# Performance work log

Measured on AMD Instinct MI355X. Metric: run time of the kernel, lower is better.

The kernel has to match this reference:

```python
import jax, jax.numpy as jnp
import numpy as np

N = 50000      # nodes
E = 640000     # edges (before self loops)
IN = 128       # in_channels
H = 4          # heads (layer 1)
C = 64         # hidden_channels per head
OUT = 64       # out_channels
SLOPE = 0.2    # PyG GATConv default negative_slope


def setup_inputs() -> dict:
    key = jax.random.key(0)
    ks = jax.random.split(key, 12)
    x = jax.random.normal(ks[0], (N, IN), dtype=jnp.float32)
    edge_src = jax.random.randint(ks[1], (E,), 0, N, dtype=jnp.int32)
    edge_dst = jax.random.randint(ks[2], (E,), 0, N, dtype=jnp.int32)
    # Layer 1 params: Linear IN -> H*C, attention vectors a_src/a_dst [H, C], bias [H*C]
    W1 = jax.random.normal(ks[3], (IN, H * C), dtype=jnp.float32) / np.sqrt(IN)
    att_src1 = jax.random.normal(ks[4], (H, C), dtype=jnp.float32) / np.sqrt(C)
    att_dst1 = jax.random.normal(ks[5], (H, C), dtype=jnp.float32) / np.sqrt(C)
    b1 = jnp.zeros((H * C,), dtype=jnp.float32)
    # Layer 2 params: Linear H*C -> OUT, 1 head
    W2 = jax.random.normal(ks[6], (H * C, OUT), dtype=jnp.float32) / np.sqrt(H * C)
    att_src2 = jax.random.normal(ks[7], (1, OUT), dtype=jnp.float32) / np.sqrt(OUT)
    att_dst2 = jax.random.normal(ks[8], (1, OUT), dtype=jnp.float32) / np.sqrt(OUT)
    b2 = jnp.zeros((OUT,), dtype=jnp.float32)
    return {"x": x, "W1": W1, "att_src1": att_src1, "att_dst1": att_dst1, "b1": b1,
            "W2": W2, "att_src2": att_src2, "att_dst2": att_dst2, "b2": b2,
            "edge_src": edge_src, "edge_dst": edge_dst}


def gat_conv(x, src, dst, W, a_src, a_dst, b, heads, ch):
    """PyG GATConv (concat=True): gather -> LeakyReLU attention -> per-dst softmax -> scatter-add."""
    n = x.shape[0]
    h = (x @ W).reshape(n, heads, ch)                  # [N, H, C]
    al_s = jnp.sum(h * a_src, axis=-1)                 # [N, H] node-level src attention term
    al_d = jnp.sum(h * a_dst, axis=-1)                 # [N, H]
    e = jax.nn.leaky_relu(al_s[src] + al_d[dst], SLOPE)  # [E, H] edge scores
    m = jax.ops.segment_max(e, dst, num_segments=n)    # stable per-dst softmax
    ex = jnp.exp(e - m[dst])
    den = jax.ops.segment_sum(ex, dst, num_segments=n)
    alpha = ex / den[dst]                              # [E, H]
    msg = h[src] * alpha[:, :, None]                   # [E, H, C]
    out = jax.ops.segment_sum(msg, dst, num_segments=n)  # [N, H, C]
    return out.reshape(n, heads * ch) + b


def reference(x, W1, att_src1, att_dst1, b1, W2, att_src2, att_dst2, b2, edge_src, edge_dst):
    # PyG GATConv default add_self_loops=True
    loops = jnp.arange(N, dtype=edge_src.dtype)
    src = jnp.concatenate([edge_src, loops])
    dst = jnp.concatenate([edge_dst, loops])
    h = gat_conv(x, src, dst, W1, att_src1, att_dst1, b1, H, C)
    h = jax.nn.elu(h)                                  # F.elu; dropout p=0 -> no-op
    out = gat_conv(h, src, dst, W2, att_src2, att_dst2, b2, 1, OUT)
    return out
```

## Files before the change

kernel.cpp:

```cpp
#include <hip/hip_runtime.h>
#include <hip/hip_bf16.h>
#include <cstdint>
#include <cstddef>

#define N_NODES 50000
#define N_EDGES 640000
#define ET (N_EDGES + N_NODES)
#define IN_CH 128
#define H1 4
#define HC1 256
#define OUT_CH 64
#define SLOPE 0.2f
#define SCAN_NBLK ((N_NODES + 255) / 256)
#define XW (N_NODES * IN_CH / 8)
#define W1N (IN_CH * HC1)
#define W2N (HC1 * OUT_CH)
#define CONVB ((XW + W1N + W2N + 255) / 256)
#define EDGEB ((ET + 255) / 256)
#define MT ((N_NODES + 63) / 64)
#define G1B (2 * MT)

typedef __attribute__((ext_vector_type(8))) short short8;
typedef __attribute__((ext_vector_type(4))) float floatx4;

__device__ __forceinline__ float bf2f(unsigned short u) {
    return __uint_as_float(((unsigned)u) << 16);
}
__device__ __forceinline__ unsigned short f2bf(float f) {
    unsigned u = __float_as_uint(f);
    unsigned r = 0x7fffu + ((u >> 16) & 1u);
    return (unsigned short)((u + r) >> 16);
}
__device__ __forceinline__ float ldf(const void* p, size_t i, bool f32) {
    return f32 ? ((const float*)p)[i] : bf2f(((const unsigned short*)p)[i]);
}
#define BLO(u) __uint_as_float((u) << 16)
#define BHI(u) __uint_as_float((u) & 0xffff0000u)

__device__ __forceinline__ bool probe_f32(const unsigned short* x) {
    int t = threadIdx.x & 63;
    int bad = 0;
    #pragma unroll
    for (int r = 0; r < 4; ++r) {
        float v = bf2f(x[r * 64 + t]);
        if (!(v == v) || fabsf(v) > 1e4f) bad = 1;
    }
    unsigned long long m = __ballot(bad != 0);
    return m != 0ull;
}

__global__ __launch_bounds__(256) void conv_count(
    const void* __restrict__ x, const void* __restrict__ W1,
    const void* __restrict__ W2, unsigned* __restrict__ flag,
    unsigned short* __restrict__ x16,
    unsigned short* __restrict__ Wt1, unsigned short* __restrict__ Wt2,
    const int* __restrict__ edst, int* __restrict__ counts,
    int* __restrict__ epos)
{
    int b = blockIdx.x;
    if (b < CONVB) {
        const bool f32 = probe_f32((const unsigned short*)x);
        if (b == 0 && threadIdx.x == 0) *flag = f32 ? 1u : 0u;
        int i = b * 256 + threadIdx.x;
        if (i < XW) {
            size_t off = (size_t)i * 8;
            uint4 st;
            if (f32) {
                const float* xp = (const float*)x + off;
                float4 a = *(const float4*)xp;
                float4 c = *(const float4*)(xp + 4);
                st.x = (unsigned)f2bf(a.x) | ((unsigned)f2bf(a.y) << 16);
                st.y = (unsigned)f2bf(a.z) | ((unsigned)f2bf(a.w) << 16);
                st.z = (unsigned)f2bf(c.x) | ((unsigned)f2bf(c.y) << 16);
                st.w = (unsigned)f2bf(c.z) | ((unsigned)f2bf(c.w) << 16);
            } else {
                st = *(const uint4*)((const unsigned short*)x + off);
            }
            *(uint4*)(x16 + off) = st;
        } else if (i < XW + W1N) {
            int j = i - XW;
            int n = j / IN_CH, k = j % IN_CH;
            Wt1[j] = f2bf(ldf(W1, (size_t)k * HC1 + n, f32));
        } else if (i < XW + W1N + W2N) {
            int j = i - XW - W1N;
            int n = j / HC1, k = j % HC1;
            Wt2[j] = f2bf(ldf(W2, (size_t)k * OUT_CH + n, f32));
        }
    } else {
        int i = (b - CONVB) * 256 + threadIdx.x;
        if (i < ET) {
            int d = (i < N_EDGES) ? edst[i] : (i - N_EDGES);
            epos[i] = atomicAdd(&counts[d], 1);
        }
    }
}

template <int KK, int NSUB>
__device__ __forceinline__ void gemm_body(
    const unsigned short* __restrict__ A, const unsigned short* __restrict__ Bt,
    const void* __restrict__ avs, const void* __restrict__ avd,
    const unsigned* __restrict__ flag, unsigned short* __restrict__ C,
    float* __restrict__ als, float* __restrict__ ald,
    int M, int N, int bx, int by)
{
    const int tid = threadIdx.x;
    const int m0 = by * 64, n0 = bx * (NSUB * 16);
    const int w = tid >> 6, lane = tid & 63;
    const int ln = lane & 15, quad = lane >> 4;
    const int m_frag = m0 + w * 16 + ln;
    floatx4 acc[NSUB];
    #pragma unroll
    for (int sub = 0; sub < NSUB; ++sub)
        acc[sub] = (floatx4){0.f, 0.f, 0.f, 0.f};

    for (int ks = 0; ks < KK / 32; ++ks) {
        const int kbase = ks * 32 + quad * 8;
        short8 a;
        if (m_frag < M) {
            a = *(const short8*)(A + (size_t)m_frag * KK + kbase);
        } else {
            #pragma unroll
            for (int j = 0; j < 8; ++j) a[j] = 0;
        }
        #pragma unroll
        for (int sub = 0; sub < NSUB; ++sub) {
            short8 b = *(const short8*)(Bt + (size_t)(n0 + sub * 16 + ln) * KK + kbase);
            acc[sub] = __builtin_amdgcn_mfma_f32_16x16x32_bf16(a, b, acc[sub], 0, 0, 0);
        }
    }

    #pragma unroll
    for (int sub = 0; sub < NSUB; ++sub) {
        #pragma unroll
        for (int r = 0; r < 4; ++r) {
            int m = m0 + w * 16 + quad * 4 + r;
            if (m < M)
                C[(size_t)m * N + n0 + sub * 16 + ln] = f2bf(acc[sub][r]);
        }
    }

    const bool f32in = (*flag != 0);
    float as[NSUB], av[NSUB];
    #pragma unroll
    for (int sub = 0; sub < NSUB; ++sub) {
        as[sub] = ldf(avs, n0 + sub * 16 + ln, f32in);
        av[sub] = ldf(avd, n0 + sub * 16 + ln, f32in);
    }
    const int Hh = N >> 6;
    #pragma unroll
    for (int hb = 0; hb < NSUB / 4; ++hb) {
        #pragma unroll
        for (int r = 0; r < 4; ++r) {
            float ps = 0.f, pd = 0.f;
            #pragma unroll
            for (int k = 0; k < 4; ++k) {
                ps += acc[hb * 4 + k][r] * as[hb * 4 + k];
                pd += acc[hb * 4 + k][r] * av[hb * 4 + k];
            }
            #pragma unroll
            for (int off = 1; off < 16; off <<= 1) {
                ps += __shfl_xor(ps, off, 64);
                pd += __shfl_xor(pd, off, 64);
            }
            int m = m0 + w * 16 + quad * 4 + r;
            if (ln == 0 && m < M) {
                als[(size_t)m * Hh + bx * (NSUB / 4) + hb] = ps;
                ald[(size_t)m * Hh + bx * (NSUB / 4) + hb] = pd;
            }
        }
    }
}

__global__ __launch_bounds__(256) void gemm1_scan_fill(
    const int* __restrict__ counts, int* __restrict__ rowptr,
    int* __restrict__ bsum, int* __restrict__ boff, int* __restrict__ state,
    const unsigned short* __restrict__ x16, const unsigned short* __restrict__ Wt1,
    const void* __restrict__ as1, const void* __restrict__ ad1,
    const unsigned* __restrict__ flag, unsigned short* __restrict__ h16,
    float* __restrict__ als, float* __restrict__ ald,
    const int* __restrict__ esrc, const int* __restrict__ edst,
    const int* __restrict__ epos, int* __restrict__ ecsr)
{
    const int b = blockIdx.x;
    const int t = threadIdx.x;
    if (b < SCAN_NBLK) {
        __shared__ int s[256];
        const int i = b * 256 + t;
        int v = (i < N_NODES) ? counts[i] : 0;
        s[t] = v;
        __syncthreads();
        #pragma unroll
        for (int off = 1; off < 256; off <<= 1) {
            int u = (t >= off) ? s[t - off] : 0;
            __syncthreads();
            s[t] += u;
            __syncthreads();
        }
        const int incl = s[t];
        if (t == 255) {
            __hip_atomic_store(&bsum[b], incl, __ATOMIC_RELAXED, __HIP_MEMORY_SCOPE_AGENT);
            __hip_atomic_fetch_add(&state[0], 1, __ATOMIC_ACQ_REL, __HIP_MEMORY_SCOPE_AGENT);
        }
        if (b == 0) {
            if (t == 0) {
                while (__hip_atomic_load(&state[0], __ATOMIC_ACQUIRE, __HIP_MEMORY_SCOPE_AGENT) < SCAN_NBLK)
                    __builtin_amdgcn_s_sleep(8);
            }
            __syncthreads();
            int w = (t < SCAN_NBLK)
                  ? __hip_atomic_load(&bsum[t], __ATOMIC_RELAXED, __HIP_MEMORY_SCOPE_AGENT) : 0;
            s[t] = w;
            __syncthreads();
            #pragma unroll
            for (int off = 1; off < 256; off <<= 1) {
                int u = (t >= off) ? s[t - off] : 0;
                __syncthreads();
                s[t] += u;
                __syncthreads();
            }
            if (t < SCAN_NBLK)
                __hip_atomic_store(&boff[t], s[t] - w, __ATOMIC_RELAXED, __HIP_MEMORY_SCOPE_AGENT);
            __syncthreads();
            if (t == 0)
                __hip_atomic_store(&state[1], 1, __ATOMIC_RELEASE, __HIP_MEMORY_SCOPE_AGENT);
        }
        if (t == 0) {
            while (__hip_atomic_load(&state[1], __ATOMIC_ACQUIRE, __HIP_MEMORY_SCOPE_AGENT) == 0)
                __builtin_amdgcn_s_sleep(8);
        }
        __syncthreads();
        int off0 = __hip_atomic_load(&boff[b], __ATOMIC_RELAXED, __HIP_MEMORY_SCOPE_AGENT);
        if (i < N_NODES)
            __hip_atomic_store(&rowptr[i], off0 + incl - v,
                               __ATOMIC_RELAXED, __HIP_MEMORY_SCOPE_AGENT);
        if (i == N_NODES - 1)
            __hip_atomic_store(&rowptr[N_NODES], off0 + incl,
                               __ATOMIC_RELAXED, __HIP_MEMORY_SCOPE_AGENT);
        __syncthreads();
        if (t == 0)
            __hip_atomic_fetch_add(&state[2], 1, __ATOMIC_ACQ_REL, __HIP_MEMORY_SCOPE_AGENT);
    } else if (b < SCAN_NBLK + G1B) {
        int g = b - SCAN_NBLK;
        gemm_body<IN_CH, 8>(x16, Wt1, as1, ad1, flag, h16, als, ald,
                            N_NODES, HC1, g & 1, g >> 1);
    } else {
        if (t == 0) {
            while (__hip_atomic_load(&state[2], __ATOMIC_ACQUIRE, __HIP_MEMORY_SCOPE_AGENT) < SCAN_NBLK)
                __builtin_amdgcn_s_sleep(8);
        }
        __syncthreads();
        int i = (b - SCAN_NBLK - G1B) * 256 + t;
        if (i < ET) {
            int s = (i < N_EDGES) ? esrc[i] : (i - N_EDGES);
            int d = (i < N_EDGES) ? edst[i] : (i - N_EDGES);
            int rp = __hip_atomic_load(&rowptr[d], __ATOMIC_RELAXED, __HIP_MEMORY_SCOPE_AGENT);
            ecsr[rp + epos[i]] = s;
        }
    }
}

__global__ __launch_bounds__(256) void agg_node1(
    const int* __restrict__ rowptr, const int* __restrict__ ecsr,
    const unsigned short* __restrict__ h, const float* __restrict__ als,
    const float* __restrict__ ald, const void* __restrict__ bias,
    const unsigned* __restrict__ flag, unsigned short* __restrict__ out)
{
    int wave = (blockIdx.x * blockDim.x + threadIdx.x) >> 6;
    int lane = threadIdx.x & 63;
    if (wave >= N_NODES) return;
    const int d = wave;
    const int hg = lane >> 4;
    const int c0 = (lane & 15) << 2;
    const int hoff = hg * 64 + c0;
    const int lo = rowptr[d], hi = rowptr[d + 1];
    const float ad = ald[d * H1 + hg];

    float acc0 = 0.f, acc1 = 0.f, acc2 = 0.f, acc3 = 0.f, den = 0.f;

    for (int e = lo; e < hi; e += 4) {
        int e1 = min(e + 1, hi - 1), e2 = min(e + 2, hi - 1), e3 = min(e + 3, hi - 1);
        int s0 = ecsr[e],  s1 = ecsr[e1], s2 = ecsr[e2], s3 = ecsr[e3];
        float t0 = als[s0 * H1 + hg] + ad;
        float t1 = als[s1 * H1 + hg] + ad;
        float t2 = als[s2 * H1 + hg] + ad;
        float t3 = als[s3 * H1 + hg] + ad;
        uint2 q0 = *(const uint2*)(h + (size_t)s0 * HC1 + hoff);
        uint2 q1 = *(const uint2*)(h + (size_t)s1 * HC1 + hoff);
        uint2 q2 = *(const uint2*)(h + (size_t)s2 * HC1 + hoff);
        uint2 q3 = *(const uint2*)(h + (size_t)s3 * HC1 + hoff);
        float p0 = __expf(fmaxf(t0, SLOPE * t0));
        float p1 = (e + 1 < hi) ? __expf(fmaxf(t1, SLOPE * t1)) : 0.f;
        float p2 = (e + 2 < hi) ? __expf(fmaxf(t2, SLOPE * t2)) : 0.f;
        float p3 = (e + 3 < hi) ? __expf(fmaxf(t3, SLOPE * t3)) : 0.f;
        den += (p0 + p1) + (p2 + p3);
        acc0 += p0 * BLO(q0.x) + p1 * BLO(q1.x) + p2 * BLO(q2.x) + p3 * BLO(q3.x);
        acc1 += p0 * BHI(q0.x) + p1 * BHI(q1.x) + p2 * BHI(q2.x) + p3 * BHI(q3.x);
        acc2 += p0 * BLO(q0.y) + p1 * BLO(q1.y) + p2 * BLO(q2.y) + p3 * BLO(q3.y);
        acc3 += p0 * BHI(q0.y) + p1 * BHI(q1.y) + p2 * BHI(q2.y) + p3 * BHI(q3.y);
    }

    const bool f32in = (*flag != 0);
    const float inv = 1.f / den;
    float v0 = acc0 * inv + ldf(bias, hoff + 0, f32in);
    float v1 = acc1 * inv + ldf(bias, hoff + 1, f32in);
    float v2 = acc2 * inv + ldf(bias, hoff + 2, f32in);
    float v3 = acc3 * inv + ldf(bias, hoff + 3, f32in);
    v0 = (v0 > 0.f) ? v0 : (__expf(v0) - 1.f);
    v1 = (v1 > 0.f) ? v1 : (__expf(v1) - 1.f);
    v2 = (v2 > 0.f) ? v2 : (__expf(v2) - 1.f);
    v3 = (v3 > 0.f) ? v3 : (__expf(v3) - 1.f);
    uint2 st;
    st.x = (unsigned)f2bf(v0) | ((unsigned)f2bf(v1) << 16);
    st.y = (unsigned)f2bf(v2) | ((unsigned)f2bf(v3) << 16);
    *(uint2*)(out + (size_t)d * HC1 + hoff) = st;
}

__global__ __launch_bounds__(256) void gemm2(
    const unsigned short* __restrict__ xo16, const unsigned short* __restrict__ Wt2,
    const void* __restrict__ as2, const void* __restrict__ ad2,
    const unsigned* __restrict__ flag, unsigned short* __restrict__ h2,
    float* __restrict__ als, float* __restrict__ ald)
{
    gemm_body<HC1, 4>(xo16, Wt2, as2, ad2, flag, h2, als, ald,
                      N_NODES, OUT_CH, 0, blockIdx.x);
}

__global__ __launch_bounds__(256) void agg_node2(
    const int* __restrict__ rowptr, const int* __restrict__ ecsr,
    const unsigned short* __restrict__ h, const float* __restrict__ als,
    const float* __restrict__ ald, const void* __restrict__ bias,
    const unsigned* __restrict__ flag, float* __restrict__ out)
{
    int wave = (blockIdx.x * blockDim.x + threadIdx.x) >> 6;
    int lane = threadIdx.x & 63;
    if (wave >= N_NODES) return;
    const int d = wave;
    const int eg = lane >> 3;
    const int c0 = (lane & 7) << 3;
    const int lo = rowptr[d], hi = rowptr[d + 1];
    const float ad = ald[d];

    float acc[8];
    #pragma unroll
    for (int j = 0; j < 8; ++j) acc[j] = 0.f;
    float den = 0.f;

    for (int eb = lo; eb < hi; eb += 8) {
        int e = eb + eg;
        if (e < hi) {
            int s = ecsr[e];
            uint4 q = *(const uint4*)(h + (size_t)s * OUT_CH + c0);
            float t = als[s] + ad;
            float p = __expf(fmaxf(t, SLOPE * t));
            den += p;
            acc[0] += p * BLO(q.x);
            acc[1] += p * BHI(q.x);
            acc[2] += p * BLO(q.y);
            acc[3] += p * BHI(q.y);
            acc[4] += p * BLO(q.z);
            acc[5] += p * BHI(q.z);
            acc[6] += p * BLO(q.w);
            acc[7] += p * BHI(q.w);
        }
    }
    #pragma unroll
    for (int off = 8; off <= 32; off <<= 1) {
        den += __shfl_xor(den, off, 64);
        #pragma unroll
        for (int j = 0; j < 8; ++j) acc[j] += __shfl_xor(acc[j], off, 64);
    }
    if (lane < 8) {
        const bool f32in = (*flag != 0);
        const float inv = 1.f / den;
        float4 v0, v1;
        v0.x = acc[0] * inv + ldf(bias, c0 + 0, f32in);
        v0.y = acc[1] * inv + ldf(bias, c0 + 1, f32in);
        v0.z = acc[2] * inv + ldf(bias, c0 + 2, f32in);
        v0.w = acc[3] * inv + ldf(bias, c0 + 3, f32in);
        v1.x = acc[4] * inv + ldf(bias, c0 + 4, f32in);
        v1.y = acc[5] * inv + ldf(bias, c0 + 5, f32in);
        v1.z = acc[6] * inv + ldf(bias, c0 + 6, f32in);
        v1.w = acc[7] * inv + ldf(bias, c0 + 7, f32in);
        *(float4*)(out + (size_t)d * OUT_CH + c0) = v0;
        *(float4*)(out + (size_t)d * OUT_CH + c0 + 4) = v1;
    }
}

extern "C" void kernel_launch(void* const* d_in, const int* in_sizes, int n_in,
                              void* d_out, int out_size, void* d_ws, size_t ws_size,
                              hipStream_t stream)
{
    const void* x   = d_in[0];
    const void* W1  = d_in[1];
    const void* as1 = d_in[2];
    const void* ad1 = d_in[3];
    const void* b1  = d_in[4];
    const void* W2  = d_in[5];
    const void* as2 = d_in[6];
    const void* ad2 = d_in[7];
    const void* b2  = d_in[8];
    const int* esrc = (const int*)d_in[9];
    const int* edst = (const int*)d_in[10];
    float* out = (float*)d_out;

    char* base = (char*)d_ws;
    const size_t MB = 1024 * 1024;
    unsigned short* x16  = (unsigned short*)(base);
    unsigned short* h16  = (unsigned short*)(base + 13 * MB);
    unsigned short* xo16 = (unsigned short*)(base + 39 * MB);
    unsigned short* h2   = (unsigned short*)(base + 65 * MB);
    float* als1   = (float*)(base + 72 * MB);
    float* ald1   = (float*)(base + 73 * MB);
    float* als2   = (float*)(base + 74 * MB);
    float* ald2   = (float*)(base + 74 * MB + 512 * 1024);
    unsigned short* Wt1 = (unsigned short*)(base + 75 * MB);
    unsigned short* Wt2 = (unsigned short*)(base + 75 * MB + 128 * 1024);
    int* counts   = (int*)(base + 76 * MB);
    int* state    = counts + N_NODES;
    int* rowptr   = (int*)(base + 77 * MB);
    int* bsum     = (int*)(base + 78 * MB);
    int* boff     = bsum + 256;
    unsigned* flag = (unsigned*)(base + 78 * MB + 8 * 1024);
    int* epos     = (int*)(base + 79 * MB);
    int* ecsr     = (int*)(base + 82 * MB);

    const int BLK = 256;
    const int node_wave_blocks = (N_NODES * 64 + BLK - 1) / BLK;

    hipMemsetAsync(counts, 0, (size_t)N_NODES * 4 + 12, stream);

    conv_count<<<CONVB + EDGEB, BLK, 0, stream>>>(
        x, W1, W2, flag, x16, Wt1, Wt2, edst, counts, epos);

    gemm1_scan_fill<<<SCAN_NBLK + G1B + EDGEB, BLK, 0, stream>>>(
        counts, rowptr, bsum, boff, state, x16, Wt1, as1, ad1, flag,
        h16, als1, ald1, esrc, edst, epos, ecsr);

    agg_node1<<<node_wave_blocks, BLK, 0, stream>>>(
        rowptr, ecsr, h16, als1, ald1, b1, flag, xo16);

    gemm2<<<MT, BLK, 0, stream>>>(xo16, Wt2, as2, ad2, flag, h2, als2, ald2);

    agg_node2<<<node_wave_blocks, BLK, 0, stream>>>(
        rowptr, ecsr, h2, als2, ald2, b2, flag, out);
}
```

Baseline: 296.8 us.

## Split scan into own kernel, narrow GEMM1 tiles, unroll layer-1 aggregation by eight

The prefix scan moves out of the fused GEMM1/fill kernel into its own launch, so the edge-fill blocks no longer spin-wait on a device-wide flag and can read rowptr with plain loads. GEMM1 tiles now cover four 64-column groups instead of two, which doubles the block count and gives each block fewer accumulators. The layer-1 aggregation loop handles eight edges per iteration with all gathers issued first, exposing more memory parallelism. The cost is one more kernel launch, a smaller GEMM tile that loses some reuse of the A tile, and higher register pressure in the aggregation loop.

Measured after the change: 293.7 us. Within noise of the previous version (-1.0%).

```diff
diff --git a/kernel.cpp b/kernel.cpp
--- a/kernel.cpp
+++ b/kernel.cpp
@@ -18,7 +18,7 @@
 #define CONVB ((XW + W1N + W2N + 255) / 256)
 #define EDGEB ((ET + 255) / 256)
 #define MT ((N_NODES + 63) / 64)
-#define G1B (2 * MT)
+#define G1B (4 * MT)
 
 typedef __attribute__((ext_vector_type(8))) short short8;
 typedef __attribute__((ext_vector_type(4))) float floatx4;
@@ -95,6 +95,62 @@
     }
 }
 
+__global__ __launch_bounds__(256) void scan_onepass(
+    const int* __restrict__ counts, int* __restrict__ rowptr,
+    int* __restrict__ bsum, int* __restrict__ boff, int* __restrict__ state)
+{
+    __shared__ int s[256];
+    const int t = threadIdx.x, b = blockIdx.x;
+    const int i = b * 256 + t;
+    int v = (i < N_NODES) ? counts[i] : 0;
+    s[t] = v;
+    __syncthreads();
+    #pragma unroll
+    for (int off = 1; off < 256; off <<= 1) {
+        int u = (t >= off) ? s[t - off] : 0;
+        __syncthreads();
+        s[t] += u;
+        __syncthreads();
+    }
+    const int incl = s[t];
+    if (t == 255) {
+        __hip_atomic_store(&bsum[b], incl, __ATOMIC_RELAXED, __HIP_MEMORY_SCOPE_AGENT);
+        __hip_atomic_fetch_add(&state[0], 1, __ATOMIC_ACQ_REL, __HIP_MEMORY_SCOPE_AGENT);
+    }
+    if (b == 0) {
+        if (t == 0) {
+            while (__hip_atomic_load(&state[0], __ATOMIC_ACQUIRE, __HIP_MEMORY_SCOPE_AGENT) < SCAN_NBLK)
+                __builtin_amdgcn_s_sleep(8);
+        }
+        __syncthreads();
+        int w = (t < SCAN_NBLK)
+              ? __hip_atomic_load(&bsum[t], __ATOMIC_RELAXED, __HIP_MEMORY_SCOPE_AGENT) : 0;
+        s[t] = w;
+        __syncthreads();
+        #pragma unroll
+        for (int off = 1; off < 256; off <<= 1) {
+            int u = (t >= off) ? s[t - off] : 0;
+            __syncthreads();
+            s[t] += u;
+            __syncthreads();
+        }
+        if (t < SCAN_NBLK)
+            __hip_atomic_store(&boff[t], s[t] - w, __ATOMIC_RELAXED, __HIP_MEMORY_SCOPE_AGENT);
+        __syncthreads();
+        if (t == 0)
+            __hip_atomic_store(&state[1], 1, __ATOMIC_RELEASE, __HIP_MEMORY_SCOPE_AGENT);
+    }
+    if (t == 0) {
+        while (__hip_atomic_load(&state[1], __ATOMIC_ACQUIRE, __HIP_MEMORY_SCOPE_AGENT) == 0)
+            __builtin_amdgcn_s_sleep(8);
+    }
+    __syncthreads();
+    int off0 = __hip_atomic_load(&boff[b], __ATOMIC_RELAXED, __HIP_MEMORY_SCOPE_AGENT);
+    if (i < N_NODES)
+        rowptr[i] = off0 + incl - v;
+    if (i == N_NODES - 1) rowptr[N_NODES] = off0 + incl;
+}
+
 template <int KK, int NSUB>
 __device__ __forceinline__ void gemm_body(
     const unsigned short* __restrict__ A, const unsigned short* __restrict__ Bt,
@@ -171,90 +227,25 @@
     }
 }
 
-__global__ __launch_bounds__(256) void gemm1_scan_fill(
-    const int* __restrict__ counts, int* __restrict__ rowptr,
-    int* __restrict__ bsum, int* __restrict__ boff, int* __restrict__ state,
+__global__ __launch_bounds__(256) void gemm1_fill(
     const unsigned short* __restrict__ x16, const unsigned short* __restrict__ Wt1,
     const void* __restrict__ as1, const void* __restrict__ ad1,
     const unsigned* __restrict__ flag, unsigned short* __restrict__ h16,
     float* __restrict__ als, float* __restrict__ ald,
     const int* __restrict__ esrc, const int* __restrict__ edst,
-    const int* __restrict__ epos, int* __restrict__ ecsr)
-{
-    const int b = blockIdx.x;
-    const int t = threadIdx.x;
-    if (b < SCAN_NBLK) {
-        __shared__ int s[256];
-        const int i = b * 256 + t;
-        int v = (i < N_NODES) ? counts[i] : 0;
-        s[t] = v;
-        __syncthreads();
-        #pragma unroll
-        for (int off = 1; off < 256; off <<= 1) {
-            int u = (t >= off) ? s[t - off] : 0;
-            __syncthreads();
-            s[t] += u;
-            __syncthreads();
-        }
-        const int incl = s[t];
-        if (t == 255) {
-            __hip_atomic_store(&bsum[b], incl, __ATOMIC_RELAXED, __HIP_MEMORY_SCOPE_AGENT);
-            __hip_atomic_fetch_add(&state[0], 1, __ATOMIC_ACQ_REL, __HIP_MEMORY_SCOPE_AGENT);
-        }
-        if (b == 0) {
-            if (t == 0) {
-                while (__hip_atomic_load(&state[0], __ATOMIC_ACQUIRE, __HIP_MEMORY_SCOPE_AGENT) < SCAN_NBLK)
-                    __builtin_amdgcn_s_sleep(8);
-            }
-            __syncthreads();
-            int w = (t < SCAN_NBLK)
-                  ? __hip_atomic_load(&bsum[t], __ATOMIC_RELAXED, __HIP_MEMORY_SCOPE_AGENT) : 0;
-            s[t] = w;
-            __syncthreads();
-            #pragma unroll
-            for (int off = 1; off < 256; off <<= 1) {
-                int u = (t >= off) ? s[t - off] : 0;
-                __syncthreads();
-                s[t] += u;
-                __syncthreads();
-            }
-            if (t < SCAN_NBLK)
-                __hip_atomic_store(&boff[t], s[t] - w, __ATOMIC_RELAXED, __HIP_MEMORY_SCOPE_AGENT);
-            __syncthreads();
-            if (t == 0)
-                __hip_atomic_store(&state[1], 1, __ATOMIC_RELEASE, __HIP_MEMORY_SCOPE_AGENT);
-        }
-        if (t == 0) {
-            while (__hip_atomic_load(&state[1], __ATOMIC_ACQUIRE, __HIP_MEMORY_SCOPE_AGENT) == 0)
-                __builtin_amdgcn_s_sleep(8);
-        }
-        __syncthreads();
-        int off0 = __hip_atomic_load(&boff[b], __ATOMIC_RELAXED, __HIP_MEMORY_SCOPE_AGENT);
-        if (i < N_NODES)
-            __hip_atomic_store(&rowptr[i], off0 + incl - v,
-                               __ATOMIC_RELAXED, __HIP_MEMORY_SCOPE_AGENT);
-        if (i == N_NODES - 1)
-            __hip_atomic_store(&rowptr[N_NODES], off0 + incl,
-                               __ATOMIC_RELAXED, __HIP_MEMORY_SCOPE_AGENT);
-        __syncthreads();
-        if (t == 0)
-            __hip_atomic_fetch_add(&state[2], 1, __ATOMIC_ACQ_REL, __HIP_MEMORY_SCOPE_AGENT);
-    } else if (b < SCAN_NBLK + G1B) {
-        int g = b - SCAN_NBLK;
-        gemm_body<IN_CH, 8>(x16, Wt1, as1, ad1, flag, h16, als, ald,
-                            N_NODES, HC1, g & 1, g >> 1);
+    const int* __restrict__ rowptr, const int* __restrict__ epos,
+    int* __restrict__ ecsr)
+{
+    int b = blockIdx.x;
+    if (b < G1B) {
+        gemm_body<IN_CH, 4>(x16, Wt1, as1, ad1, flag, h16, als, ald,
+                            N_NODES, HC1, b & 3, b >> 2);
     } else {
-        if (t == 0) {
-            while (__hip_atomic_load(&state[2], __ATOMIC_ACQUIRE, __HIP_MEMORY_SCOPE_AGENT) < SCAN_NBLK)
-                __builtin_amdgcn_s_sleep(8);
-        }
-        __syncthreads();
-        int i = (b - SCAN_NBLK - G1B) * 256 + t;
+        int i = (b - G1B) * 256 + threadIdx.x;
         if (i < ET) {
             int s = (i < N_EDGES) ? esrc[i] : (i - N_EDGES);
             int d = (i < N_EDGES) ? edst[i] : (i - N_EDGES);
-            int rp = __hip_atomic_load(&rowptr[d], __ATOMIC_RELAXED, __HIP_MEMORY_SCOPE_AGENT);
-            ecsr[rp + epos[i]] = s;
+            ecsr[rowptr[d] + epos[i]] = s;
         }
     }
 }
@@ -277,26 +268,46 @@
 
     float acc0 = 0.f, acc1 = 0.f, acc2 = 0.f, acc3 = 0.f, den = 0.f;
 
-    for (int e = lo; e < hi; e += 4) {
-        int e1 = min(e + 1, hi - 1), e2 = min(e + 2, hi - 1), e3 = min(e + 3, hi - 1);
+    for (int e = lo; e < hi; e += 8) {
+        int e1 = min(e + 1, hi - 1), e2 = min(e + 2, hi - 1);
+        int e3 = min(e + 3, hi - 1), e4 = min(e + 4, hi - 1);
+        int e5 = min(e + 5, hi - 1), e6 = min(e + 6, hi - 1);
+        int e7 = min(e + 7, hi - 1);
         int s0 = ecsr[e],  s1 = ecsr[e1], s2 = ecsr[e2], s3 = ecsr[e3];
+        int s4 = ecsr[e4], s5 = ecsr[e5], s6 = ecsr[e6], s7 = ecsr[e7];
+        uint2 q0 = *(const uint2*)(h + (size_t)s0 * HC1 + hoff);
+        uint2 q1 = *(const uint2*)(h + (size_t)s1 * HC1 + hoff);
+        uint2 q2 = *(const uint2*)(h + (size_t)s2 * HC1 + hoff);
+        uint2 q3 = *(const uint2*)(h + (size_t)s3 * HC1 + hoff);
+        uint2 q4 = *(const uint2*)(h + (size_t)s4 * HC1 + hoff);
+        uint2 q5 = *(const uint2*)(h + (size_t)s5 * HC1 + hoff);
+        uint2 q6 = *(const uint2*)(h + (size_t)s6 * HC1 + hoff);
+        uint2 q7 = *(const uint2*)(h + (size_t)s7 * HC1 + hoff);
         float t0 = als[s0 * H1 + hg] + ad;
         float t1 = als[s1 * H1 + hg] + ad;
         float t2 = als[s2 * H1 + hg] + ad;
         float t3 = als[s3 * H1 + hg] + ad;
-        uint2 q0 = *(const uint2*)(h + (size_t)s0 * HC1 + hoff);
-        uint2 q1 = *(const uint2*)(h + (size_t)s1 * HC1 + hoff);
-        uint2 q2 = *(const uint2*)(h + (size_t)s2 * HC1 + hoff);
-        uint2 q3 = *(const uint2*)(h + (size_t)s3 * HC1 + hoff);
+        float t4 = als[s4 * H1 + hg] + ad;
+        float t5 = als[s5 * H1 + hg] + ad;
+        float t6 = als[s6 * H1 + hg] + ad;
+        float t7 = als[s7 * H1 + hg] + ad;
         float p0 = __expf(fmaxf(t0, SLOPE * t0));
         float p1 = (e + 1 < hi) ? __expf(fmaxf(t1, SLOPE * t1)) : 0.f;
         float p2 = (e + 2 < hi) ? __expf(fmaxf(t2, SLOPE * t2)) : 0.f;
         float p3 = (e + 3 < hi) ? __expf(fmaxf(t3, SLOPE * t3)) : 0.f;
-        den += (p0 + p1) + (p2 + p3);
-        acc0 += p0 * BLO(q0.x) + p1 * BLO(q1.x) + p2 * BLO(q2.x) + p3 * BLO(q3.x);
-        acc1 += p0 * BHI(q0.x) + p1 * BHI(q1.x) + p2 * BHI(q2.x) + p3 * BHI(q3.x);
-        acc2 += p0 * BLO(q0.y) + p1 * BLO(q1.y) + p2 * BLO(q2.y) + p3 * BLO(q3.y);
-        acc3 += p0 * BHI(q0.y) + p1 * BHI(q1.y) + p2 * BHI(q2.y) + p3 * BHI(q3.y);
+        float p4 = (e + 4 < hi) ? __expf(fmaxf(t4, SLOPE * t4)) : 0.f;
+        float p5 = (e + 5 < hi) ? __expf(fmaxf(t5, SLOPE * t5)) : 0.f;
+        float p6 = (e + 6 < hi) ? __expf(fmaxf(t6, SLOPE * t6)) : 0.f;
+        float p7 = (e + 7 < hi) ? __expf(fmaxf(t7, SLOPE * t7)) : 0.f;
+        den += ((p0 + p1) + (p2 + p3)) + ((p4 + p5) + (p6 + p7));
+        acc0 += p0 * BLO(q0.x) + p1 * BLO(q1.x) + p2 * BLO(q2.x) + p3 * BLO(q3.x)
+              + p4 * BLO(q4.x) + p5 * BLO(q5.x) + p6 * BLO(q6.x) + p7 * BLO(q7.x);
+        acc1 += p0 * BHI(q0.x) + p1 * BHI(q1.x) + p2 * BHI(q2.x) + p3 * BHI(q3.x)
+              + p4 * BHI(q4.x) + p5 * BHI(q5.x) + p6 * BHI(q6.x) + p7 * BHI(q7.x);
+        acc2 += p0 * BLO(q0.y) + p1 * BLO(q1.y) + p2 * BLO(q2.y) + p3 * BLO(q3.y)
+              + p4 * BLO(q4.y) + p5 * BLO(q5.y) + p6 * BLO(q6.y) + p7 * BLO(q7.y);
+        acc3 += p0 * BHI(q0.y) + p1 * BHI(q1.y) + p2 * BHI(q2.y) + p3 * BHI(q3.y)
+              + p4 * BHI(q4.y) + p5 * BHI(q5.y) + p6 * BHI(q6.y) + p7 * BHI(q7.y);
     }
 
     const bool f32in = (*flag != 0);
@@ -432,9 +443,12 @@
     conv_count<<<CONVB + EDGEB, BLK, 0, stream>>>(
         x, W1, W2, flag, x16, Wt1, Wt2, edst, counts, epos);
 
-    gemm1_scan_fill<<<SCAN_NBLK + G1B + EDGEB, BLK, 0, stream>>>(
-        counts, rowptr, bsum, boff, state, x16, Wt1, as1, ad1, flag,
-        h16, als1, ald1, esrc, edst, epos, ecsr);
+    scan_onepass<<<SCAN_NBLK, BLK, 0, stream>>>(
+        counts, rowptr, bsum, boff, state);
+
+    gemm1_fill<<<G1B + EDGEB, BLK, 0, stream>>>(
+        x16, Wt1, as1, ad1, flag, h16, als1, ald1, esrc, edst, rowptr, epos,
+        ecsr);
 
     agg_node1<<<node_wave_blocks, BLK, 0, stream>>>(
         rowptr, ecsr, h16, als1, ald1, b1, flag, xo16);
```
